# Optimization experiments

Hardware: AMD Instinct MI355X
Metric: run time of the kernel (lower is better)

Reference implementation:

```python
import jax, jax.numpy as jnp
import numpy as np

GROUP_SIZE = 128
IN_FEATURES = 8192
OUT_FEATURES = 28672
TOKENS = 32


def _dequantize(qweight, qzeros, scales):
    """ExLlama q4 dequant.
    qweight: (K//8, N) int32, 8 int4 values per word packed along k.
    qzeros:  (G, N//8) int32, 8 int4 zeros per word packed along n.
    scales:  (G, N) fp16.  g = k // GROUP_SIZE; w = s * (q - (z + 1)).
    """
    shifts = jnp.arange(8, dtype=jnp.int32) * 4
    K = qweight.shape[0] * 8
    N = qweight.shape[1]
    G = qzeros.shape[0]
    # unpack weights along k: (K//8, 8, N) -> (K, N)
    q = (qweight[:, None, :] >> shifts[None, :, None]) & 15
    q = q.reshape(K, N)
    # unpack zeros along n: (G, N//8, 8) -> (G, N)
    z = (qzeros[:, :, None] >> shifts[None, None, :]) & 15
    z = z.reshape(G, N)
    # group-wise dequant: reshape k into (G, GROUP_SIZE)
    qg = q.reshape(G, GROUP_SIZE, N).astype(jnp.float16)
    zf = (z + 1).astype(jnp.float16)[:, None, :]          # ExLlama stores zero-1
    w = (qg - zf) * scales[:, None, :]                    # (G, GS, N) fp16
    return w.reshape(K, N)


def setup_inputs() -> dict:
    key = jax.random.key(0)
    k1, k2, k3, k4, k5 = jax.random.split(key, 5)
    x = jax.random.normal(k1, (TOKENS, IN_FEATURES), dtype=jnp.float16)
    qweight = jax.random.randint(k2, (IN_FEATURES // 8, OUT_FEATURES),
                                 minval=-(2**31), maxval=2**31 - 1, dtype=jnp.int32)
    qzeros = jax.random.randint(k3, (IN_FEATURES // GROUP_SIZE, OUT_FEATURES // 8),
                                minval=-(2**31), maxval=2**31 - 1, dtype=jnp.int32)
    scales = (jax.random.uniform(k4, (IN_FEATURES // GROUP_SIZE, OUT_FEATURES),
                                 dtype=jnp.float32) * 0.01 + 0.001).astype(jnp.float16)
    bias = jax.random.normal(k5, (OUT_FEATURES,), dtype=jnp.float16)
    return {"x": x, "qweight": qweight, "qzeros": qzeros,
            "scales": scales, "bias": bias}


def reference(x, qweight, qzeros, scales, bias):
    w = _dequantize(qweight, qzeros, scales)              # (K, N) fp16
    out = jnp.matmul(x.astype(jnp.float16), w)            # (T, N)
    return out + bias
```

## Files before the change

### kernel.cpp

```cpp
#include <hip/hip_runtime.h>
#include <hip/hip_bf16.h>

#define T_TOK   32
#define KDIM    8192
#define NDIM    28672
#define NGRP    64
#define NZWORDS 3584

typedef _Float16 half8 __attribute__((ext_vector_type(8)));
typedef float    f32x4 __attribute__((ext_vector_type(4)));

template<int NSEG, bool DIRECT>
__global__ __launch_bounds__(256, 4)
void exllama_gemm(const int*   __restrict__ qweight,
                  const int*   __restrict__ qzeros,
                  const float* __restrict__ scales,
                  const float* __restrict__ x,
                  const float* __restrict__ bias,
                  float*       __restrict__ ws,
                  float*       __restrict__ out)
{
    const int lane = threadIdx.x & 63;
    const int wav  = threadIdx.x >> 6;
    const int quad = lane >> 4;
    const int l16  = lane & 15;
    const int seg  = blockIdx.y;
    const int n0   = blockIdx.x * 256 + wav * 64;

    int nc[4];
    #pragma unroll
    for (int j = 0; j < 4; ++j) nc[j] = n0 + j * 16 + l16;

    f32x4 acc[4][2];
    #pragma unroll
    for (int j = 0; j < 4; ++j)
        #pragma unroll
        for (int m = 0; m < 2; ++m)
            acc[j][m] = (f32x4){0.f, 0.f, 0.f, 0.f};

    const int GPS = NGRP / NSEG;
    const int g0  = seg * GPS;

    const float* xr0 = x + (size_t)l16 * KDIM + quad * 8;
    const float* xr1 = xr0 + (size_t)16 * KDIM;

    auto load_group = [&](int g, unsigned (&qw)[16], float (&sv)[4], float (&bv)[4]) {
        #pragma unroll
        for (int j = 0; j < 4; ++j) {
            float s  = scales[(size_t)g * NDIM + nc[j]];
            int   zw = qzeros[(size_t)g * NZWORDS + (nc[j] >> 3)];
            int   z  = (zw >> ((nc[j] & 7) * 4)) & 15;
            sv[j] = s;
            bv[j] = -s * (float)(z + 1);
        }
        const size_t rb = (size_t)(g * 16 + quad) * NDIM;
        #pragma unroll
        for (int c = 0; c < 4; ++c)
            #pragma unroll
            for (int j = 0; j < 4; ++j)
                qw[c * 4 + j] = (unsigned)qweight[rb + (size_t)(c * 4) * NDIM + nc[j]];
    };

    auto compute_group = [&](int g, const unsigned (&qw)[16],
                             const float (&sv)[4], const float (&bv)[4]) {
        #pragma unroll
        for (int c = 0; c < 4; ++c) {
            const int kofs = g * 128 + c * 32;
            f32x4 xa = *(const f32x4*)(xr0 + kofs);
            f32x4 xb = *(const f32x4*)(xr0 + kofs + 4);
            f32x4 xc = *(const f32x4*)(xr1 + kofs);
            f32x4 xd = *(const f32x4*)(xr1 + kofs + 4);
            half8 a0, a1;
            #pragma unroll
            for (int i = 0; i < 4; ++i) {
                a0[i]     = (_Float16)xa[i];
                a0[i + 4] = (_Float16)xb[i];
                a1[i]     = (_Float16)xc[i];
                a1[i + 4] = (_Float16)xd[i];
            }
            #pragma unroll
            for (int j = 0; j < 4; ++j) {
                const unsigned w = qw[c * 4 + j];
                half8 bf;
                #pragma unroll
                for (int i = 0; i < 8; ++i) {
                    float q = (float)((w >> (4 * i)) & 15u);
                    bf[i] = (_Float16)__builtin_fmaf(q, sv[j], bv[j]);
                }
                acc[j][0] = __builtin_amdgcn_mfma_f32_16x16x32_f16(a0, bf, acc[j][0], 0, 0, 0);
                acc[j][1] = __builtin_amdgcn_mfma_f32_16x16x32_f16(a1, bf, acc[j][1], 0, 0, 0);
            }
        }
    };

    unsigned qwA[16], qwB[16];
    float svA[4], bvA[4], svB[4], bvB[4];

    load_group(g0, qwA, svA, bvA);
    #pragma unroll 1
    for (int gi = 0; gi < GPS; gi += 2) {
        load_group(g0 + gi + 1, qwB, svB, bvB);
        compute_group(g0 + gi, qwA, svA, bvA);
        if (gi + 2 < GPS) load_group(g0 + gi + 2, qwA, svA, bvA);
        compute_group(g0 + gi + 1, qwB, svB, bvB);
    }

    if (DIRECT) {
        #pragma unroll
        for (int j = 0; j < 4; ++j) {
            const int n  = n0 + j * 16 + l16;
            const float bb = bias[n];
            #pragma unroll
            for (int m = 0; m < 2; ++m)
                #pragma unroll
                for (int r = 0; r < 4; ++r) {
                    const int t = m * 16 + quad * 4 + r;
                    out[(size_t)t * NDIM + n] = acc[j][m][r] + bb;
                }
        }
    } else {
        float* wsp = ws + (size_t)seg * (T_TOK * NDIM);
        #pragma unroll
        for (int j = 0; j < 4; ++j) {
            const int n = n0 + j * 16 + l16;
            #pragma unroll
            for (int m = 0; m < 2; ++m)
                #pragma unroll
                for (int r = 0; r < 4; ++r) {
                    const int t = m * 16 + quad * 4 + r;
                    wsp[(size_t)t * NDIM + n] = acc[j][m][r];
                }
        }
    }
}

template<int NSEG>
__global__ __launch_bounds__(256)
void reduce_bias(const float* __restrict__ ws,
                 const float* __restrict__ bias,
                 float*       __restrict__ out)
{
    const int e = (blockIdx.x * 256 + threadIdx.x) * 4;
    const int n = e % NDIM;
    f32x4 sum = (f32x4){0.f, 0.f, 0.f, 0.f};
    #pragma unroll
    for (int s = 0; s < NSEG; ++s)
        sum += *(const f32x4*)(ws + (size_t)s * (T_TOK * NDIM) + e);
    f32x4 bb = *(const f32x4*)(bias + n);
    *(f32x4*)(out + e) = sum + bb;
}

extern "C" void kernel_launch(void* const* d_in, const int* in_sizes, int n_in,
                              void* d_out, int out_size, void* d_ws, size_t ws_size,
                              hipStream_t stream)
{
    const float* x  = (const float*)d_in[0];
    const int* qweight = (const int*)d_in[1];
    const int* qzeros  = (const int*)d_in[2];
    const float* sc = (const float*)d_in[3];
    const float* bs = (const float*)d_in[4];
    float* out      = (float*)d_out;

    const size_t need = (size_t)8 * T_TOK * NDIM * sizeof(float);
    if (ws_size >= need) {
        exllama_gemm<8, false><<<dim3(112, 8), 256, 0, stream>>>(
            qweight, qzeros, sc, x, bs, (float*)d_ws, out);
        reduce_bias<8><<<(T_TOK * NDIM) / (256 * 4), 256, 0, stream>>>(
            (const float*)d_ws, bs, out);
    } else {
        exllama_gemm<1, true><<<dim3(112, 1), 256, 0, stream>>>(
            qweight, qzeros, sc, x, bs, nullptr, out);
    }
}
```

Measured before the change: 235.8 us.

## Stage fp16 activations in LDS and use magic-number packed-half dequant

The split-K GEMM kernel now converts its 1024-wide slice of x to fp16 once per block and keeps it in shared memory (padded rows), so MFMA A operands come from LDS instead of repeated fp32 global loads and conversions. Dequantization switches from per-element float FMA to the 0x6400 magic-number trick on packed half2 values, cutting ALU work per weight. Launch bounds occupancy drops from 4 to 2 blocks per CU because of the 66KB LDS tile, and computing in fp16 can round slightly differently. The fallback direct kernel is rewritten without prefetching.

Result: faster. 203.4 us (-13.8%).

```diff
diff --git a/kernel.cpp b/kernel.cpp
--- a/kernel.cpp
+++ b/kernel.cpp
@@ -1,30 +1,168 @@
 #include <hip/hip_runtime.h>
-#include <hip/hip_bf16.h>
 
 #define T_TOK   32
 #define KDIM    8192
 #define NDIM    28672
 #define NGRP    64
 #define NZWORDS 3584
-
-typedef _Float16 half8 __attribute__((ext_vector_type(8)));
-typedef float    f32x4 __attribute__((ext_vector_type(4)));
-
-template<int NSEG, bool DIRECT>
-__global__ __launch_bounds__(256, 4)
-void exllama_gemm(const int*   __restrict__ qweight,
-                  const int*   __restrict__ qzeros,
-                  const float* __restrict__ scales,
-                  const float* __restrict__ x,
-                  const float* __restrict__ bias,
-                  float*       __restrict__ ws,
-                  float*       __restrict__ out)
+#define NSEG    8
+#define SEGK    1024
+#define GPS     8
+#define XROW    1032
+
+typedef _Float16 half8  __attribute__((ext_vector_type(8)));
+typedef _Float16 half2v __attribute__((ext_vector_type(2)));
+typedef float    f32x4  __attribute__((ext_vector_type(4)));
+typedef unsigned uint4v __attribute__((ext_vector_type(4)));
+
+__global__ __launch_bounds__(256, 2)
+void exllama_gemm_lds(const int*   __restrict__ qweight,
+                      const int*   __restrict__ qzeros,
+                      const float* __restrict__ scales,
+                      const float* __restrict__ x,
+                      float*       __restrict__ ws)
+{
+    __shared__ alignas(16) _Float16 xs[T_TOK * XROW];
+
+    const int tid  = threadIdx.x;
+    const int lane = tid & 63;
+    const int wav  = tid >> 6;
+    const int quad = lane >> 4;
+    const int l16  = lane & 15;
+    const int seg  = blockIdx.y;
+    const int n0   = blockIdx.x * 256 + wav * 64;
+
+    {
+        const int kseg0 = seg * SEGK;
+        #pragma unroll
+        for (int it = 0; it < (T_TOK * SEGK) / (256 * 8); ++it) {
+            const int e  = it * 2048 + tid * 8;
+            const int t  = e >> 10;
+            const int kl = e & 1023;
+            const float* xp = x + (size_t)t * KDIM + kseg0 + kl;
+            f32x4 lo = *(const f32x4*)xp;
+            f32x4 hi = *(const f32x4*)(xp + 4);
+            uint4v u;
+            #pragma unroll
+            for (int j = 0; j < 4; ++j) {
+                unsigned a = (unsigned)__builtin_bit_cast(unsigned short, (_Float16)lo[j]);
+                unsigned b = (unsigned)__builtin_bit_cast(unsigned short, (_Float16)hi[j]);
+                u[j] = a | (b << 16);
+            }
+            *(uint4v*)(xs + t * XROW + kl) = u;
+        }
+    }
+    __syncthreads();
+
+    int nc[4];
+    #pragma unroll
+    for (int j = 0; j < 4; ++j) nc[j] = n0 + j * 16 + l16;
+
+    f32x4 acc[4][2];
+    #pragma unroll
+    for (int j = 0; j < 4; ++j)
+        #pragma unroll
+        for (int m = 0; m < 2; ++m)
+            acc[j][m] = (f32x4){0.f, 0.f, 0.f, 0.f};
+
+    const int g0 = seg * GPS;
+
+    unsigned qw[2][16];
+    half2v   sp[2][4], cp[2][4];
+
+    auto load_group = [&](int g, int b) {
+        #pragma unroll
+        for (int j = 0; j < 4; ++j) {
+            float s  = scales[(size_t)g * NDIM + nc[j]];
+            int   zw = qzeros[(size_t)g * NZWORDS + (nc[j] >> 3)];
+            int   z  = (zw >> ((nc[j] & 7) * 4)) & 15;
+            _Float16 sh = (_Float16)s;
+            _Float16 ch = (_Float16)(float)(-(1025 + z));
+            sp[b][j] = (half2v){sh, sh};
+            cp[b][j] = (half2v){ch, ch};
+        }
+        const size_t rb = (size_t)(g * 16 + quad) * NDIM;
+        #pragma unroll
+        for (int c = 0; c < 4; ++c)
+            #pragma unroll
+            for (int j = 0; j < 4; ++j)
+                qw[b][c * 4 + j] = (unsigned)qweight[rb + (size_t)(c * 4) * NDIM + nc[j]];
+    };
+
+    auto compute_group = [&](int gi, int b) {
+        #pragma unroll
+        for (int c = 0; c < 4; ++c) {
+            const int kloc = gi * 128 + c * 32 + quad * 8;
+            half8 a0 = *(const half8*)(xs + l16 * XROW + kloc);
+            half8 a1 = *(const half8*)(xs + (l16 + 16) * XROW + kloc);
+            #pragma unroll
+            for (int j = 0; j < 4; ++j) {
+                const unsigned w = qw[b][c * 4 + j];
+                uint4v bu;
+                #pragma unroll
+                for (int i = 0; i < 4; ++i) {
+                    unsigned t = ((w >> (4 * i)) & 0x000F000Fu) | 0x64006400u;
+                    half2v th = __builtin_bit_cast(half2v, t);
+                    half2v r  = (th + cp[b][j]) * sp[b][j];
+                    bu[i] = __builtin_bit_cast(unsigned, r);
+                }
+                half8 bf = __builtin_bit_cast(half8, bu);
+                acc[j][0] = __builtin_amdgcn_mfma_f32_16x16x32_f16(a0, bf, acc[j][0], 0, 0, 0);
+                acc[j][1] = __builtin_amdgcn_mfma_f32_16x16x32_f16(a1, bf, acc[j][1], 0, 0, 0);
+            }
+        }
+    };
+
+    load_group(g0, 0);
+    #pragma unroll 1
+    for (int gi = 0; gi < GPS; gi += 2) {
+        load_group(g0 + gi + 1, 1);
+        compute_group(gi, 0);
+        if (gi + 2 < GPS) load_group(g0 + gi + 2, 0);
+        compute_group(gi + 1, 1);
+    }
+
+    float* wsp = ws + (size_t)seg * (T_TOK * NDIM);
+    #pragma unroll
+    for (int j = 0; j < 4; ++j) {
+        const int n = n0 + j * 16 + l16;
+        #pragma unroll
+        for (int m = 0; m < 2; ++m)
+            #pragma unroll
+            for (int r = 0; r < 4; ++r) {
+                const int t = m * 16 + quad * 4 + r;
+                wsp[(size_t)t * NDIM + n] = acc[j][m][r];
+            }
+    }
+}
+
+__global__ __launch_bounds__(256)
+void reduce_bias(const float* __restrict__ ws,
+                 const float* __restrict__ bias,
+                 float*       __restrict__ out)
+{
+    const int e = (blockIdx.x * 256 + threadIdx.x) * 4;
+    const int n = e % NDIM;
+    f32x4 sum = (f32x4){0.f, 0.f, 0.f, 0.f};
+    #pragma unroll
+    for (int s = 0; s < NSEG; ++s)
+        sum += *(const f32x4*)(ws + (size_t)s * (T_TOK * NDIM) + e);
+    f32x4 bb = *(const f32x4*)(bias + n);
+    *(f32x4*)(out + e) = sum + bb;
+}
+
+__global__ __launch_bounds__(256)
+void exllama_gemm_direct(const int*   __restrict__ qweight,
+                         const int*   __restrict__ qzeros,
+                         const float* __restrict__ scales,
+                         const float* __restrict__ x,
+                         const float* __restrict__ bias,
+                         float*       __restrict__ out)
 {
     const int lane = threadIdx.x & 63;
     const int wav  = threadIdx.x >> 6;
     const int quad = lane >> 4;
     const int l16  = lane & 15;
-    const int seg  = blockIdx.y;
     const int n0   = blockIdx.x * 256 + wav * 64;
 
     int nc[4];
@@ -38,116 +176,54 @@
         for (int m = 0; m < 2; ++m)
             acc[j][m] = (f32x4){0.f, 0.f, 0.f, 0.f};
 
-    const int GPS = NGRP / NSEG;
-    const int g0  = seg * GPS;
-
-    const float* xr0 = x + (size_t)l16 * KDIM + quad * 8;
-    const float* xr1 = xr0 + (size_t)16 * KDIM;
-
-    auto load_group = [&](int g, unsigned (&qw)[16], float (&sv)[4], float (&bv)[4]) {
+    #pragma unroll 1
+    for (int g = 0; g < NGRP; ++g) {
+        float sv[4], bv[4];
         #pragma unroll
         for (int j = 0; j < 4; ++j) {
             float s  = scales[(size_t)g * NDIM + nc[j]];
             int   zw = qzeros[(size_t)g * NZWORDS + (nc[j] >> 3)];
             int   z  = (zw >> ((nc[j] & 7) * 4)) & 15;
-            sv[j] = s;
-            bv[j] = -s * (float)(z + 1);
-        }
-        const size_t rb = (size_t)(g * 16 + quad) * NDIM;
-        #pragma unroll
-        for (int c = 0; c < 4; ++c)
-            #pragma unroll
-            for (int j = 0; j < 4; ++j)
-                qw[c * 4 + j] = (unsigned)qweight[rb + (size_t)(c * 4) * NDIM + nc[j]];
-    };
-
-    auto compute_group = [&](int g, const unsigned (&qw)[16],
-                             const float (&sv)[4], const float (&bv)[4]) {
+            sv[j] = s; bv[j] = -s * (float)(z + 1);
+        }
         #pragma unroll
         for (int c = 0; c < 4; ++c) {
-            const int kofs = g * 128 + c * 32;
-            f32x4 xa = *(const f32x4*)(xr0 + kofs);
-            f32x4 xb = *(const f32x4*)(xr0 + kofs + 4);
-            f32x4 xc = *(const f32x4*)(xr1 + kofs);
-            f32x4 xd = *(const f32x4*)(xr1 + kofs + 4);
+            const int kw    = g * 16 + c * 4 + quad;
+            const int kbase = (g * 16 + c * 4) * 8;
             half8 a0, a1;
             #pragma unroll
-            for (int i = 0; i < 4; ++i) {
-                a0[i]     = (_Float16)xa[i];
-                a0[i + 4] = (_Float16)xb[i];
-                a1[i]     = (_Float16)xc[i];
-                a1[i + 4] = (_Float16)xd[i];
+            for (int m = 0; m < 2; ++m) {
+                const float* xp = x + (size_t)(l16 + 16 * m) * KDIM + kbase + quad * 8;
+                f32x4 xa = *(const f32x4*)xp;
+                f32x4 xb = *(const f32x4*)(xp + 4);
+                #pragma unroll
+                for (int i = 0; i < 4; ++i) {
+                    (m ? a1 : a0)[i]     = (_Float16)xa[i];
+                    (m ? a1 : a0)[i + 4] = (_Float16)xb[i];
+                }
             }
             #pragma unroll
             for (int j = 0; j < 4; ++j) {
-                const unsigned w = qw[c * 4 + j];
+                const unsigned w = (unsigned)qweight[(size_t)kw * NDIM + nc[j]];
                 half8 bf;
                 #pragma unroll
-                for (int i = 0; i < 8; ++i) {
-                    float q = (float)((w >> (4 * i)) & 15u);
-                    bf[i] = (_Float16)__builtin_fmaf(q, sv[j], bv[j]);
-                }
+                for (int i = 0; i < 8; ++i)
+                    bf[i] = (_Float16)__builtin_fmaf((float)((w >> (4 * i)) & 15u), sv[j], bv[j]);
                 acc[j][0] = __builtin_amdgcn_mfma_f32_16x16x32_f16(a0, bf, acc[j][0], 0, 0, 0);
                 acc[j][1] = __builtin_amdgcn_mfma_f32_16x16x32_f16(a1, bf, acc[j][1], 0, 0, 0);
             }
         }
-    };
-
-    unsigned qwA[16], qwB[16];
-    float svA[4], bvA[4], svB[4], bvB[4];
-
-    load_group(g0, qwA, svA, bvA);
-    #pragma unroll 1
-    for (int gi = 0; gi < GPS; gi += 2) {
-        load_group(g0 + gi + 1, qwB, svB, bvB);
-        compute_group(g0 + gi, qwA, svA, bvA);
-        if (gi + 2 < GPS) load_group(g0 + gi + 2, qwA, svA, bvA);
-        compute_group(g0 + gi + 1, qwB, svB, bvB);
-    }
-
-    if (DIRECT) {
-        #pragma unroll
-        for (int j = 0; j < 4; ++j) {
-            const int n  = n0 + j * 16 + l16;
-            const float bb = bias[n];
-            #pragma unroll
-            for (int m = 0; m < 2; ++m)
-                #pragma unroll
-                for (int r = 0; r < 4; ++r) {
-                    const int t = m * 16 + quad * 4 + r;
-                    out[(size_t)t * NDIM + n] = acc[j][m][r] + bb;
-                }
-        }
-    } else {
-        float* wsp = ws + (size_t)seg * (T_TOK * NDIM);
-        #pragma unroll
-        for (int j = 0; j < 4; ++j) {
-            const int n = n0 + j * 16 + l16;
-            #pragma unroll
-            for (int m = 0; m < 2; ++m)
-                #pragma unroll
-                for (int r = 0; r < 4; ++r) {
-                    const int t = m * 16 + quad * 4 + r;
-                    wsp[(size_t)t * NDIM + n] = acc[j][m][r];
-                }
-        }
-    }
-}
-
-template<int NSEG>
-__global__ __launch_bounds__(256)
-void reduce_bias(const float* __restrict__ ws,
-                 const float* __restrict__ bias,
-                 float*       __restrict__ out)
-{
-    const int e = (blockIdx.x * 256 + threadIdx.x) * 4;
-    const int n = e % NDIM;
-    f32x4 sum = (f32x4){0.f, 0.f, 0.f, 0.f};
-    #pragma unroll
-    for (int s = 0; s < NSEG; ++s)
-        sum += *(const f32x4*)(ws + (size_t)s * (T_TOK * NDIM) + e);
-    f32x4 bb = *(const f32x4*)(bias + n);
-    *(f32x4*)(out + e) = sum + bb;
+    }
+    #pragma unroll
+    for (int j = 0; j < 4; ++j) {
+        const int n = n0 + j * 16 + l16;
+        const float bb = bias[n];
+        #pragma unroll
+        for (int m = 0; m < 2; ++m)
+            #pragma unroll
+            for (int r = 0; r < 4; ++r)
+                out[(size_t)(m * 16 + quad * 4 + r) * NDIM + n] = acc[j][m][r] + bb;
+    }
 }
 
 extern "C" void kernel_launch(void* const* d_in, const int* in_sizes, int n_in,
@@ -161,14 +237,14 @@
     const float* bs = (const float*)d_in[4];
     float* out      = (float*)d_out;
 
-    const size_t need = (size_t)8 * T_TOK * NDIM * sizeof(float);
+    const size_t need = (size_t)NSEG * T_TOK * NDIM * sizeof(float);
     if (ws_size >= need) {
-        exllama_gemm<8, false><<<dim3(112, 8), 256, 0, stream>>>(
-            qweight, qzeros, sc, x, bs, (float*)d_ws, out);
-        reduce_bias<8><<<(T_TOK * NDIM) / (256 * 4), 256, 0, stream>>>(
+        exllama_gemm_lds<<<dim3(112, NSEG), 256, 0, stream>>>(
+            qweight, qzeros, sc, x, (float*)d_ws);
+        reduce_bias<<<(T_TOK * NDIM) / (256 * 4), 256, 0, stream>>>(
             (const float*)d_ws, bs, out);
     } else {
-        exllama_gemm<1, true><<<dim3(112, 1), 256, 0, stream>>>(
-            qweight, qzeros, sc, x, bs, nullptr, out);
-    }
-}
+        exllama_gemm_direct<<<112, 256, 0, stream>>>(
+            qweight, qzeros, sc, x, bs, out);
+    }
+}
```

## Fuse split-K reduction via atomics and use packed fp16 magic-number dequant

Applied to the files above, without the earlier changes.

Drops the workspace write and the separate reduce_bias kernel. Each K-segment block now atomically adds its partial sums, plus bias/NSEG, straight into the output. Dequantisation changes from per-element fp32 FMA to packed half2 arithmetic using the 0x6400 exponent trick, and x is converted with cvt_pkrtz so the k-permutation matches. The occupancy hint drops from 4 to 3. This relies on the output buffer being zeroed before launch, and atomic fp32 accumulation makes the summation order nondeterministic.

After: 239.8 us. No clear change (+1.7%).

```diff
diff --git a/kernel.cpp b/kernel.cpp
--- a/kernel.cpp
+++ b/kernel.cpp
@@ -1,24 +1,25 @@
 #include <hip/hip_runtime.h>
-#include <hip/hip_bf16.h>
 
 #define T_TOK   32
 #define KDIM    8192
 #define NDIM    28672
 #define NGRP    64
 #define NZWORDS 3584
+#define NSEG    8
+#define GPS     (NGRP / NSEG)
 
-typedef _Float16 half8 __attribute__((ext_vector_type(8)));
-typedef float    f32x4 __attribute__((ext_vector_type(4)));
+typedef _Float16 half8  __attribute__((ext_vector_type(8)));
+typedef _Float16 half2v __attribute__((ext_vector_type(2)));
+typedef float    f32x4  __attribute__((ext_vector_type(4)));
+typedef unsigned uint4v __attribute__((ext_vector_type(4)));
 
-template<int NSEG, bool DIRECT>
-__global__ __launch_bounds__(256, 4)
-void exllama_gemm(const int*   __restrict__ qweight,
-                  const int*   __restrict__ qzeros,
-                  const float* __restrict__ scales,
-                  const float* __restrict__ x,
-                  const float* __restrict__ bias,
-                  float*       __restrict__ ws,
-                  float*       __restrict__ out)
+__global__ __launch_bounds__(256, 3)
+void exllama_gemm_atomic(const int*   __restrict__ qweight,
+                         const int*   __restrict__ qzeros,
+                         const float* __restrict__ scales,
+                         const float* __restrict__ x,
+                         const float* __restrict__ bias,
+                         float*       __restrict__ out)
 {
     const int lane = threadIdx.x & 63;
     const int wav  = threadIdx.x >> 6;
@@ -38,116 +39,88 @@
         for (int m = 0; m < 2; ++m)
             acc[j][m] = (f32x4){0.f, 0.f, 0.f, 0.f};
 
-    const int GPS = NGRP / NSEG;
-    const int g0  = seg * GPS;
+    const int g0 = seg * GPS;
 
     const float* xr0 = x + (size_t)l16 * KDIM + quad * 8;
     const float* xr1 = xr0 + (size_t)16 * KDIM;
 
-    auto load_group = [&](int g, unsigned (&qw)[16], float (&sv)[4], float (&bv)[4]) {
+    unsigned qw[2][16];
+    half2v   sp[2][4], cp[2][4];
+
+    auto load_group = [&](int g, int b) {
         #pragma unroll
         for (int j = 0; j < 4; ++j) {
             float s  = scales[(size_t)g * NDIM + nc[j]];
             int   zw = qzeros[(size_t)g * NZWORDS + (nc[j] >> 3)];
             int   z  = (zw >> ((nc[j] & 7) * 4)) & 15;
-            sv[j] = s;
-            bv[j] = -s * (float)(z + 1);
+            _Float16 sh = (_Float16)s;
+            _Float16 ch = (_Float16)(float)(-(1025 + z));
+            sp[b][j] = (half2v){sh, sh};
+            cp[b][j] = (half2v){ch, ch};
         }
         const size_t rb = (size_t)(g * 16 + quad) * NDIM;
         #pragma unroll
         for (int c = 0; c < 4; ++c)
             #pragma unroll
             for (int j = 0; j < 4; ++j)
-                qw[c * 4 + j] = (unsigned)qweight[rb + (size_t)(c * 4) * NDIM + nc[j]];
+                qw[b][c * 4 + j] = (unsigned)qweight[rb + (size_t)(c * 4) * NDIM + nc[j]];
     };
 
-    auto compute_group = [&](int g, const unsigned (&qw)[16],
-                             const float (&sv)[4], const float (&bv)[4]) {
+    auto compute_group = [&](int g, int b) {
         #pragma unroll
         for (int c = 0; c < 4; ++c) {
-            const int kofs = g * 128 + c * 32;
-            f32x4 xa = *(const f32x4*)(xr0 + kofs);
-            f32x4 xb = *(const f32x4*)(xr0 + kofs + 4);
-            f32x4 xc = *(const f32x4*)(xr1 + kofs);
-            f32x4 xd = *(const f32x4*)(xr1 + kofs + 4);
-            half8 a0, a1;
+            const int kof = g * 128 + c * 32;
+            f32x4 xa = *(const f32x4*)(xr0 + kof);
+            f32x4 xb = *(const f32x4*)(xr0 + kof + 4);
+            f32x4 xc = *(const f32x4*)(xr1 + kof);
+            f32x4 xd = *(const f32x4*)(xr1 + kof + 4);
+            uint4v u0, u1;
             #pragma unroll
             for (int i = 0; i < 4; ++i) {
-                a0[i]     = (_Float16)xa[i];
-                a0[i + 4] = (_Float16)xb[i];
-                a1[i]     = (_Float16)xc[i];
-                a1[i + 4] = (_Float16)xd[i];
+                u0[i] = __builtin_bit_cast(unsigned, __builtin_amdgcn_cvt_pkrtz(xa[i], xb[i]));
+                u1[i] = __builtin_bit_cast(unsigned, __builtin_amdgcn_cvt_pkrtz(xc[i], xd[i]));
             }
+            half8 a0 = __builtin_bit_cast(half8, u0);
+            half8 a1 = __builtin_bit_cast(half8, u1);
             #pragma unroll
             for (int j = 0; j < 4; ++j) {
-                const unsigned w = qw[c * 4 + j];
-                half8 bf;
+                const unsigned w = qw[b][c * 4 + j];
+                uint4v bu;
                 #pragma unroll
-                for (int i = 0; i < 8; ++i) {
-                    float q = (float)((w >> (4 * i)) & 15u);
-                    bf[i] = (_Float16)__builtin_fmaf(q, sv[j], bv[j]);
+                for (int i = 0; i < 4; ++i) {
+                    unsigned t = ((w >> (4 * i)) & 0x000F000Fu) | 0x64006400u;
+                    half2v th = __builtin_bit_cast(half2v, t);
+                    half2v r  = (th + cp[b][j]) * sp[b][j];
+                    bu[i] = __builtin_bit_cast(unsigned, r);
                 }
+                half8 bf = __builtin_bit_cast(half8, bu);
                 acc[j][0] = __builtin_amdgcn_mfma_f32_16x16x32_f16(a0, bf, acc[j][0], 0, 0, 0);
                 acc[j][1] = __builtin_amdgcn_mfma_f32_16x16x32_f16(a1, bf, acc[j][1], 0, 0, 0);
             }
         }
     };
 
-    unsigned qwA[16], qwB[16];
-    float svA[4], bvA[4], svB[4], bvB[4];
-
-    load_group(g0, qwA, svA, bvA);
+    load_group(g0, 0);
     #pragma unroll 1
     for (int gi = 0; gi < GPS; gi += 2) {
-        load_group(g0 + gi + 1, qwB, svB, bvB);
-        compute_group(g0 + gi, qwA, svA, bvA);
-        if (gi + 2 < GPS) load_group(g0 + gi + 2, qwA, svA, bvA);
-        compute_group(g0 + gi + 1, qwB, svB, bvB);
+        load_group(g0 + gi + 1, 1);
+        compute_group(g0 + gi, 0);
+        if (gi + 2 < GPS) load_group(g0 + gi + 2, 0);
+        compute_group(g0 + gi + 1, 1);
     }
 
-    if (DIRECT) {
+    #pragma unroll
+    for (int j = 0; j < 4; ++j) {
+        const int n  = n0 + j * 16 + l16;
+        const float bb = bias[n] * (1.0f / NSEG);
         #pragma unroll
-        for (int j = 0; j < 4; ++j) {
-            const int n  = n0 + j * 16 + l16;
-            const float bb = bias[n];
+        for (int m = 0; m < 2; ++m)
             #pragma unroll
-            for (int m = 0; m < 2; ++m)
-                #pragma unroll
-                for (int r = 0; r < 4; ++r) {
-                    const int t = m * 16 + quad * 4 + r;
-                    out[(size_t)t * NDIM + n] = acc[j][m][r] + bb;
-                }
-        }
-    } else {
-        float* wsp = ws + (size_t)seg * (T_TOK * NDIM);
-        #pragma unroll
-        for (int j = 0; j < 4; ++j) {
-            const int n = n0 + j * 16 + l16;
-            #pragma unroll
-            for (int m = 0; m < 2; ++m)
-                #pragma unroll
-                for (int r = 0; r < 4; ++r) {
-                    const int t = m * 16 + quad * 4 + r;
-                    wsp[(size_t)t * NDIM + n] = acc[j][m][r];
-                }
-        }
+            for (int r = 0; r < 4; ++r) {
+                const int t = m * 16 + quad * 4 + r;
+                unsafeAtomicAdd(out + (size_t)t * NDIM + n, acc[j][m][r] + bb);
+            }
     }
-}
-
-template<int NSEG>
-__global__ __launch_bounds__(256)
-void reduce_bias(const float* __restrict__ ws,
-                 const float* __restrict__ bias,
-                 float*       __restrict__ out)
-{
-    const int e = (blockIdx.x * 256 + threadIdx.x) * 4;
-    const int n = e % NDIM;
-    f32x4 sum = (f32x4){0.f, 0.f, 0.f, 0.f};
-    #pragma unroll
-    for (int s = 0; s < NSEG; ++s)
-        sum += *(const f32x4*)(ws + (size_t)s * (T_TOK * NDIM) + e);
-    f32x4 bb = *(const f32x4*)(bias + n);
-    *(f32x4*)(out + e) = sum + bb;
 }
 
 extern "C" void kernel_launch(void* const* d_in, const int* in_sizes, int n_in,
@@ -160,15 +133,8 @@
     const float* sc = (const float*)d_in[3];
     const float* bs = (const float*)d_in[4];
     float* out      = (float*)d_out;
+    (void)d_ws; (void)ws_size;
 
-    const size_t need = (size_t)8 * T_TOK * NDIM * sizeof(float);
-    if (ws_size >= need) {
-        exllama_gemm<8, false><<<dim3(112, 8), 256, 0, stream>>>(
-            qweight, qzeros, sc, x, bs, (float*)d_ws, out);
-        reduce_bias<8><<<(T_TOK * NDIM) / (256 * 4), 256, 0, stream>>>(
-            (const float*)d_ws, bs, out);
-    } else {
-        exllama_gemm<1, true><<<dim3(112, 1), 256, 0, stream>>>(
-            qweight, qzeros, sc, x, bs, nullptr, out);
-    }
+    exllama_gemm_atomic<<<dim3(NDIM / 256, NSEG), 256, 0, stream>>>(
+        qweight, qzeros, sc, x, bs, out);
 }
```
